# Kernel optimization log

Measured on AMD Instinct MI355X. Metric: run time of the kernel, lower is better.

## Reference

```python
import jax, jax.numpy as jnp
import numpy as np

N_U = 50000   # num user nodes
N_I = 50000   # num item nodes
D = 64        # in_size == out_size
H = 128       # SemanticAttention hidden size (default)
E = 500000    # edges per meta-path graph
NEG_SLOPE = 0.01


def setup_inputs() -> dict:
    key = jax.random.key(0)
    ks = jax.random.split(key, 24)
    rn = lambda k, shp, s=0.1: jax.random.normal(k, shp, jnp.float32) * s
    ri = lambda k, shp, n: jax.random.randint(k, shp, 0, n, dtype=jnp.int32)
    return dict(
        feat_user=rn(ks[0], (N_U, D)), feat_item=rn(ks[1], (N_I, D)),
        attn_l=rn(ks[2], (4, D)), attn_r=rn(ks[3], (4, D)),
        W_gc=rn(ks[4], (4, D, D)), b_gc=jnp.zeros((4, D), jnp.float32),
        sa_rel_W1=rn(ks[5], (D, H)), sa_rel_b1=jnp.zeros((H,), jnp.float32), sa_rel_w2=rn(ks[6], (H,)),
        sa_u_W1=rn(ks[7], (D, H)), sa_u_b1=jnp.zeros((H,), jnp.float32), sa_u_w2=rn(ks[8], (H,)),
        sa_i_W1=rn(ks[9], (D, H)), sa_i_b1=jnp.zeros((H,), jnp.float32), sa_i_w2=rn(ks[10], (H,)),
        rel_u_src=ri(ks[11], (2, E), N_I), rel_u_dst=ri(ks[12], (2, E), N_U),
        rel_i_src=ri(ks[13], (2, E), N_U), rel_i_dst=ri(ks[14], (2, E), N_I),
        mp_u_src=ri(ks[15], (2, E), N_U), mp_u_dst=ri(ks[16], (2, E), N_U),
        mp_i_src=ri(ks[17], (2, E), N_I), mp_i_dst=ri(ks[18], (2, E), N_I),
    )


def _edge_softmax(e, dst, n_dst):
    # segment-wise (per destination node) softmax over irregular edges
    m = jax.ops.segment_max(e, dst, num_segments=n_dst)
    ex = jnp.exp(e - m[dst])
    s = jax.ops.segment_sum(ex, dst, num_segments=n_dst)
    return ex / s[dst]


def _heco_gat(src, dst, feat_src, feat_dst, al, ar, n_dst):
    # HeCoGATConv: el = sum(ft_src*attn_l), er = sum(ft_dst*attn_r)
    el = feat_src @ al  # (N_src,)
    er = feat_dst @ ar  # (N_dst,)
    e = jax.nn.leaky_relu(el[src] + er[dst], NEG_SLOPE)  # (E,)
    a = _edge_softmax(e, dst, n_dst)
    out = jax.ops.segment_sum(feat_src[src] * a[:, None], dst, num_segments=n_dst)
    return jax.nn.elu(out)


def _graph_conv(src, dst, feat, W, b, n):
    # DGL GraphConv with norm='both', activation=elu
    ones = jnp.ones(src.shape, jnp.float32)
    deg_out = jax.ops.segment_sum(ones, src, num_segments=n)
    deg_in = jax.ops.segment_sum(ones, dst, num_segments=n)
    no = jnp.where(deg_out > 0, deg_out, 1.0) ** -0.5
    ni = jnp.where(deg_in > 0, deg_in, 1.0) ** -0.5
    h = feat * no[:, None]
    agg = jax.ops.segment_sum(h[src], dst, num_segments=n)
    agg = agg * ni[:, None]
    return jax.nn.elu(agg @ W + b)


def _semantic_attention(z, W1, b1, w2):
    # z: (N, M, D) -> (N, D)
    w = (jnp.tanh(z @ W1 + b1) @ w2).mean(0)  # (M,)
    beta = jax.nn.softmax(w)
    return jnp.einsum('nmd,m->nd', z, beta)


def reference(feat_user, feat_item, attn_l, attn_r, W_gc, b_gc,
              sa_rel_W1, sa_rel_b1, sa_rel_w2,
              sa_u_W1, sa_u_b1, sa_u_w2,
              sa_i_W1, sa_i_b1, sa_i_w2,
              rel_u_src, rel_u_dst, rel_i_src, rel_i_dst,
              mp_u_src, mp_u_dst, mp_i_src, mp_i_dst):
    # --- RelationalAGG: HeCo GAT over schema-level relations ---
    zu = jnp.stack([
        _heco_gat(rel_u_src[0], rel_u_dst[0], feat_item, feat_user, attn_l[0], attn_r[0], N_U),
        _heco_gat(rel_u_src[1], rel_u_dst[1], feat_item, feat_user, attn_l[1], attn_r[1], N_U),
    ], axis=1)  # (N_U, 2, D)
    rel_u = _semantic_attention(zu, sa_rel_W1, sa_rel_b1, sa_rel_w2)
    zi = jnp.stack([
        _heco_gat(rel_i_src[0], rel_i_dst[0], feat_user, feat_item, attn_l[2], attn_r[2], N_I),
        _heco_gat(rel_i_src[1], rel_i_dst[1], feat_user, feat_item, attn_l[3], attn_r[3], N_I),
    ], axis=1)
    rel_i = _semantic_attention(zi, sa_rel_W1, sa_rel_b1, sa_rel_w2)
    # --- HAN layers: GraphConv over meta-path reachable graphs ---
    hu = jnp.stack([
        _graph_conv(mp_u_src[0], mp_u_dst[0], feat_user, W_gc[0], b_gc[0], N_U),
        _graph_conv(mp_u_src[1], mp_u_dst[1], feat_user, W_gc[1], b_gc[1], N_U),
    ], axis=1)
    han_u = _semantic_attention(hu, sa_u_W1, sa_u_b1, sa_u_w2)
    hi = jnp.stack([
        _graph_conv(mp_i_src[0], mp_i_dst[0], feat_item, W_gc[2], b_gc[2], N_I),
        _graph_conv(mp_i_src[1], mp_i_dst[1], feat_item, W_gc[3], b_gc[3], N_I),
    ], axis=1)
    han_i = _semantic_attention(hi, sa_i_W1, sa_i_b1, sa_i_w2)
    user_emb = rel_u + han_u
    item_emb = rel_i + han_i
    return jnp.concatenate([user_emb, item_emb], axis=0)  # (N_U + N_I, D)
```

## Files before the change

kernel.cpp:

```cpp
#include <hip/hip_runtime.h>
#include <math.h>

#define NU 50000
#define NI 50000
#define NN 50000
#define DD 64
#define HHID 128
#define EE 500000
#define NEG_SLOPE 0.01f
#define NBKT 196
#define CAP 3072
#define TILE 8192
#define TPG 62
#define P1T 512
#define NIMG 12
#define AGGB 1563
#define SEMB 512

typedef _Float16 half_t;
typedef _Float16 half8 __attribute__((ext_vector_type(8)));
typedef float f32x4 __attribute__((ext_vector_type(4)));
union H4 { uint2 u; half_t h[4]; };
union H8 { uint4 u; half_t h[8]; };
union HS { half8 h; int i[4]; uint4 u; };
union HC { unsigned short us; half_t h; };

struct Ptr4c { const float* p[4]; };
struct Ptr4m { float*       p[4]; };
struct EdgeArgs { const int* src[8]; const int* dst[8]; };
struct GatArgs { const half_t* fsrc[4]; half_t* zout[4]; };
struct GcArgs  { const half_t* feat[4]; half_t* hout[4]; };
struct WArgs   { const float* el[4]; const float* er[4]; const int* deg_src; };
struct SemArgs { const half_t* z[4]; const float* W1[4]; const float* b1[4]; const float* w2[4]; };
struct PrepArgs {
    const float* featI; const float* featU;
    Ptr4c vi; Ptr4c vu; Ptr4m oi; Ptr4m ou;
    half_t* FBI; half_t* FBU;
    const float* W_gc; half_t* W16;
};

__global__ __launch_bounds__(256) void prep_kernel(PrepArgs pa) {
    int b = blockIdx.x;
    int t = threadIdx.x;
    if (b == 6250) {
        int g = t >> 6;
        int lane = t & 63;
        int cl = lane & 15, quad = lane >> 4;
#pragma unroll
        for (int nt = 0; nt < 4; nt++) {
#pragma unroll
            for (int kh = 0; kh < 2; kh++) {
                H8 o;
#pragma unroll
                for (int j = 0; j < 8; j++) {
                    int k = kh * 32 + quad * 8 + j;
                    int n = nt * 16 + cl;
                    o.h[j] = (half_t)pa.W_gc[g * 4096 + k * 64 + n];
                }
                *(uint4*)(pa.W16 + ((g * 8 + nt * 2 + kh) * 64 + lane) * 8) = o.u;
            }
        }
        return;
    }
    const float* feat; Ptr4c vecs; Ptr4m outs; half_t* fb16; int bb;
    if (b < 3125) { feat = pa.featI; vecs = pa.vi; outs = pa.oi; fb16 = pa.FBI; bb = b; }
    else          { feat = pa.featU; vecs = pa.vu; outs = pa.ou; fb16 = pa.FBU; bb = b - 3125; }
    int w = bb * 4 + (t >> 6);
    int lane = t & 63;
    int sub = lane >> 4, r = lane & 15;
    int node = w * 4 + sub;
    float4 f = *(const float4*)(feat + node * DD + r * 4);
    H4 o16;
    o16.h[0] = (half_t)f.x; o16.h[1] = (half_t)f.y; o16.h[2] = (half_t)f.z; o16.h[3] = (half_t)f.w;
    *(uint2*)(fb16 + node * DD + r * 4) = o16.u;
#pragma unroll
    for (int j = 0; j < 4; j++) {
        float4 vv = *(const float4*)(vecs.p[j] + r * 4);
        float val = f.x * vv.x + f.y * vv.y + f.z * vv.z + f.w * vv.w;
        val += __shfl_down(val, 8);
        val += __shfl_down(val, 4);
        val += __shfl_down(val, 2);
        val += __shfl_down(val, 1);
        if (r == 0) outs.p[j][node] = val;
    }
}

__global__ __launch_bounds__(P1T) void part1_kernel(EdgeArgs a, int* __restrict__ ccnt,
                                                    int* __restrict__ coarse) {
    __shared__ int bc_cnt[256], bc_scan[256], bc_start[256], bc_cur[256], bc_gbase[256];
    __shared__ int stage[TILE];
    int t = threadIdx.x;
    int g = blockIdx.x / TPG;
    int tile = blockIdx.x % TPG;
    int e0 = tile * TILE;
    int tile_n = min(TILE, EE - e0);
    bool cnt_only = g >= 8;
    const int* gk = (cnt_only ? a.src[g - 4] : a.dst[g]) + e0;
    const int* gs = cnt_only ? gk : (a.src[g] + e0);
    if (t < 256) bc_cnt[t] = 0;
    __syncthreads();
    for (int pos = t * 4; pos < tile_n; pos += P1T * 4) {
        int4 k4 = *(const int4*)(gk + pos);
        atomicAdd(&bc_cnt[k4.x >> 8], 1);
        atomicAdd(&bc_cnt[k4.y >> 8], 1);
        atomicAdd(&bc_cnt[k4.z >> 8], 1);
        atomicAdd(&bc_cnt[k4.w >> 8], 1);
    }
    __syncthreads();
    if (t < 256) bc_scan[t] = bc_cnt[t];
    __syncthreads();
    for (int off = 1; off < 256; off <<= 1) {
        int v = (t < 256 && t >= off) ? bc_scan[t - off] : 0;
        __syncthreads();
        if (t < 256) bc_scan[t] += v;
        __syncthreads();
    }
    if (t < 256) {
        int st = bc_scan[t] - bc_cnt[t];
        bc_start[t] = st;
        bc_cur[t] = st;
        bc_gbase[t] = (t < NBKT && bc_cnt[t] > 0) ? atomicAdd(&ccnt[g * NBKT + t], bc_cnt[t]) : 0;
    }
    __syncthreads();
    for (int pos = t * 4; pos < tile_n; pos += P1T * 4) {
        int4 k4 = *(const int4*)(gk + pos);
        int4 s4;
        if (cnt_only) { s4 = make_int4(0, 0, 0, 0); }
        else          { s4 = *(const int4*)(gs + pos); }
        int b0 = k4.x >> 8, b1 = k4.y >> 8, b2 = k4.z >> 8, b3 = k4.w >> 8;
        int sl0 = atomicAdd(&bc_cur[b0], 1);
        int sl1 = atomicAdd(&bc_cur[b1], 1);
        int sl2 = atomicAdd(&bc_cur[b2], 1);
        int sl3 = atomicAdd(&bc_cur[b3], 1);
        stage[sl0] = s4.x | ((k4.x & 255) << 16) | (b0 << 24);
        stage[sl1] = s4.y | ((k4.y & 255) << 16) | (b1 << 24);
        stage[sl2] = s4.z | ((k4.z & 255) << 16) | (b2 << 24);
        stage[sl3] = s4.w | ((k4.w & 255) << 16) | (b3 << 24);
    }
    __syncthreads();
    for (int j = t; j < tile_n; j += P1T) {
        int p = stage[j];
        int b = (unsigned)p >> 24;
        int pos = bc_gbase[b] + (j - bc_start[b]);
        if (pos < CAP) coarse[(g * NBKT + b) * CAP + pos] = p & 0x00FFFFFF;
    }
}

__global__ __launch_bounds__(256) void degcnt_kernel(const int* __restrict__ ccnt,
                                                     const int* __restrict__ coarse,
                                                     int* __restrict__ DEG_SRC) {
    __shared__ int cnt[256];
    int t = threadIdx.x;
    int g2 = blockIdx.x / NBKT;
    int b = blockIdx.x % NBKT;
    int img = 8 + g2;
    int n = min(ccnt[img * NBKT + b], CAP);
    cnt[t] = 0;
    __syncthreads();
    const int* pairs = coarse + (img * NBKT + b) * CAP;
    for (int i = t; i < n; i += 256) atomicAdd(&cnt[(pairs[i] >> 16) & 255], 1);
    __syncthreads();
    int v = (b << 8) + t;
    if (v < NN) DEG_SRC[g2 * NN + v] = cnt[t];
}

__global__ __launch_bounds__(256) void part2_kernel(const int* __restrict__ ccnt,
                                                    const int* __restrict__ coarse,
                                                    WArgs wa,
                                                    int* __restrict__ bucket,
                                                    int2* __restrict__ RD) {
    __shared__ int sb[256];
    __shared__ int cnt5[256], off5[256], s2[256];
    __shared__ int ordered[CAP];
    int t = threadIdx.x;
    int g = blockIdx.x / NBKT;
    int b = blockIdx.x % NBKT;
    int ccv = (t < NBKT) ? min(ccnt[g * NBKT + t], CAP) : 0;
    sb[t] = ccv;
    cnt5[t] = 0;
    __syncthreads();
    for (int off = 1; off < 256; off <<= 1) {
        int vv = (t >= off) ? sb[t - off] : 0;
        __syncthreads();
        sb[t] += vv;
        __syncthreads();
    }
    int base = (b > 0) ? sb[b - 1] : 0;
    int n = sb[b] - base;
    int node0 = b << 8;
    const int* pairs = coarse + (g * NBKT + b) * CAP;
    for (int i = t; i < n; i += 256) atomicAdd(&cnt5[pairs[i] >> 16], 1);
    __syncthreads();
    int myc = cnt5[t];
    s2[t] = myc;
    __syncthreads();
    for (int off = 1; off < 256; off <<= 1) {
        int vv = (t >= off) ? s2[t - off] : 0;
        __syncthreads();
        s2[t] += vv;
        __syncthreads();
    }
    int ex = s2[t] - myc;
    off5[t] = ex;
    int v = node0 + t;
    if (v < NN) RD[g * NN + v] = make_int2(base + ex, myc);
    __syncthreads();
    int nm1 = n - 1;
    for (int ib = t; ib < n; ib += 1024) {
        int p[4];
#pragma unroll
        for (int u = 0; u < 4; u++) {
            int i = ib + u * 256;
            p[u] = pairs[(i < n) ? i : nm1];
        }
        float w[4];
        if (g < 4) {
            float a0[4], a1[4];
#pragma unroll
            for (int u = 0; u < 4; u++) a0[u] = wa.el[g][p[u] & 0xFFFF];
#pragma unroll
            for (int u = 0; u < 4; u++) a1[u] = wa.er[g][node0 + (p[u] >> 16)];
#pragma unroll
            for (int u = 0; u < 4; u++) {
                float e = a0[u] + a1[u];
                e = (e >= 0.f) ? e : NEG_SLOPE * e;
                w[u] = __expf(e);
            }
        } else {
            int dv[4];
#pragma unroll
            for (int u = 0; u < 4; u++) dv[u] = wa.deg_src[(g - 4) * NN + (p[u] & 0xFFFF)];
#pragma unroll
            for (int u = 0; u < 4; u++) w[u] = __builtin_amdgcn_rsqf((float)dv[u]);
        }
#pragma unroll
        for (int u = 0; u < 4; u++) {
            int i = ib + u * 256;
            if (i < n) {
                HC cv; cv.h = (half_t)w[u];
                int slot = atomicAdd(&off5[p[u] >> 16], 1);
                ordered[slot] = (p[u] & 0xFFFF) | ((int)cv.us << 16);
            }
        }
    }
    __syncthreads();
    int* bko = bucket + g * EE + base;
    for (int i = t; i < n; i += 256) bko[i] = ordered[i];
}

__global__ __launch_bounds__(256) void agg_kernel(GatArgs ga, GcArgs gc, half_t* __restrict__ AGG,
                                                  const int2* __restrict__ RD,
                                                  const int* __restrict__ bucket) {
    int g = blockIdx.x / AGGB;
    int nb = blockIdx.x % AGGB;
    int t = threadIdx.x;
    int wv = t >> 6, lane = t & 63;
    int q = lane >> 3, r = lane & 7;
    int v = nb * 32 + wv * 8 + q;
    bool vok = v < NN;
    int2 rd = RD[g * NN + (vok ? v : 0)];
    int start = rd.x;
    int dg = vok ? rd.y : 0;
    const int* bk = bucket + g * EE;
    const half_t* feat = (g < 4) ? ga.fsrc[g] : gc.feat[g - 4];
    int roff = r << 3;
    int obase = lane & 56;
    HS acc[4];
#pragma unroll
    for (int a = 0; a < 4; a++)
#pragma unroll
        for (int j = 0; j < 4; j++) acc[a].i[j] = 0;
    float s_l = 0.f;
    for (int b8 = 0; b8 < dg; b8 += 8) {
        int rem = dg - b8;
        int p = bk[start + b8 + ((r < rem) ? r : 0)];
#pragma unroll
        for (int j = 0; j < 8; j++) {
            if (j < rem) {
                int pj = __shfl(p, obase + j);
                HC wj; wj.us = (unsigned short)((unsigned)pj >> 16);
                s_l += (float)wj.h;
                HS row; row.u = *(const uint4*)(feat + (((pj & 0xFFFF) << 6) + roff));
                half_t wh = wj.h;
                half8 ws = {wh, wh, wh, wh, wh, wh, wh, wh};
                acc[j & 3].h += row.h * ws;
            }
        }
    }
    acc[0].h += acc[1].h;
    acc[2].h += acc[3].h;
    acc[0].h += acc[2].h;
    if (g < 4) {
        float inv = (dg > 0) ? __builtin_amdgcn_rcpf(s_l) : 0.f;
        H8 o;
#pragma unroll
        for (int i = 0; i < 8; i++) {
            float x = (float)acc[0].h[i] * inv;
            x = (x > 0.f) ? x : (__expf(x) - 1.f);
            o.h[i] = (half_t)x;
        }
        if (vok) *(uint4*)(ga.zout[g] + (v << 7) + roff) = o.u;
    } else {
        float niv = (dg > 0) ? __builtin_amdgcn_rsqf((float)dg) : 1.0f;
        H8 o;
#pragma unroll
        for (int i = 0; i < 8; i++) o.h[i] = (half_t)((float)acc[0].h[i] * niv);
        if (vok) *(uint4*)(AGG + (((g - 4) * NN + v) << 6) + roff) = o.u;
    }
}

__global__ __launch_bounds__(256) void trans_kernel(GcArgs gc, const half_t* __restrict__ AGG,
                                                    const half_t* __restrict__ W16,
                                                    const float* __restrict__ b_gc) {
    int t = threadIdx.x;
    int wv = t >> 6, lane = t & 63;
    int g = blockIdx.x / 782;
    int tile = (blockIdx.x % 782) * 4 + wv;
    if (tile >= 3125) return;
    int cl = lane & 15, quad = lane >> 4;
    const half_t* ab = AGG + ((g * NN + tile * 16 + cl) << 6);
    half8 A0 = *(const half8*)(ab + quad * 8);
    half8 A1 = *(const half8*)(ab + 32 + quad * 8);
    const half_t* wbase = W16 + g * 8 * 64 * 8;
    half_t* hout = gc.hout[g];
#pragma unroll
    for (int nt = 0; nt < 4; nt++) {
        float bb = b_gc[g * 64 + nt * 16 + cl];
        f32x4 c = {bb, bb, bb, bb};
        half8 B0 = *(const half8*)(wbase + ((nt * 2 + 0) * 64 + lane) * 8);
        half8 B1 = *(const half8*)(wbase + ((nt * 2 + 1) * 64 + lane) * 8);
        c = __builtin_amdgcn_mfma_f32_16x16x32_f16(A0, B0, c, 0, 0, 0);
        c = __builtin_amdgcn_mfma_f32_16x16x32_f16(A1, B1, c, 0, 0, 0);
#pragma unroll
        for (int r_ = 0; r_ < 4; r_++) {
            int node = tile * 16 + quad * 4 + r_;
            float x = c[r_];
            x = (x > 0.f) ? x : (__expf(x) - 1.f);
            hout[node * 128 + nt * 16 + cl] = (half_t)x;
        }
    }
}

__global__ __launch_bounds__(256) void sem_att_kernel(SemArgs sa, float* __restrict__ wsum) {
    __shared__ float s0[4], s1[4];
    int inst = blockIdx.x / SEMB;
    int blk  = blockIdx.x % SEMB;
    int t = threadIdx.x;
    int wv = t >> 6, lane = t & 63;
    int quad = lane >> 4, cl = lane & 15;
    const half_t* z = sa.z[inst];
    const float* W1 = sa.W1[inst];
    half8 Bf[2][2];
    float b1v[2], w2v[2];
#pragma unroll
    for (int u = 0; u < 2; u++) {
        int nt = wv * 2 + u;
        int n = nt * 16 + cl;
#pragma unroll
        for (int kh = 0; kh < 2; kh++) {
#pragma unroll
            for (int j = 0; j < 8; j++) {
                int k = kh * 32 + quad * 8 + j;
                Bf[u][kh][j] = (half_t)W1[k * HHID + n];
            }
        }
        b1v[u] = sa.b1[inst][nt * 16 + cl];
        w2v[u] = sa.w2[inst][nt * 16 + cl];
    }
    float local0 = 0.f, local1 = 0.f;
    int tile = blk;
    half8 A0, A1, nA0, nA1;
    {
        int m = (tile >= 3125) ? 1 : 0;
        int node = (tile - m * 3125) * 16 + cl;
        const half_t* zr = z + node * 128 + m * 64 + quad * 8;
        A0 = *(const half8*)(zr);
        A1 = *(const half8*)(zr + 32);
    }
    while (tile < 6250) {
        int ntile = tile + SEMB;
        if (ntile < 6250) {
            int m = (ntile >= 3125) ? 1 : 0;
            int node = (ntile - m * 3125) * 16 + cl;
            const half_t* zr = z + node * 128 + m * 64 + quad * 8;
            nA0 = *(const half8*)(zr);
            nA1 = *(const half8*)(zr + 32);
        }
        float sumv = 0.f;
#pragma unroll
        for (int u = 0; u < 2; u++) {
            f32x4 c = {0.f, 0.f, 0.f, 0.f};
            c = __builtin_amdgcn_mfma_f32_16x16x32_f16(A0, Bf[u][0], c, 0, 0, 0);
            c = __builtin_amdgcn_mfma_f32_16x16x32_f16(A1, Bf[u][1], c, 0, 0, 0);
#pragma unroll
            for (int r = 0; r < 4; r++) {
                float xv = c[r] + b1v[u];
                float tv = __expf(2.f * xv);
                float th = 1.f - 2.f * __builtin_amdgcn_rcpf(tv + 1.f);
                sumv += th * w2v[u];
            }
        }
#pragma unroll
        for (int off = 32; off > 0; off >>= 1) sumv += __shfl_down(sumv, off);
        if (lane == 0) { if (tile < 3125) local0 += sumv; else local1 += sumv; }
        A0 = nA0; A1 = nA1;
        tile = ntile;
    }
    if (lane == 0) { s0[wv] = local0; s1[wv] = local1; }
    __syncthreads();
    if (t == 0) {
        float a0 = s0[0] + s0[1] + s0[2] + s0[3];
        float a1 = s1[0] + s1[1] + s1[2] + s1[3];
        if (a0 != 0.f) atomicAdd(&wsum[inst * 2 + 0], a0);
        if (a1 != 0.f) atomicAdd(&wsum[inst * 2 + 1], a1);
    }
}

__global__ void combine_kernel(const half_t* __restrict__ ZU, const half_t* __restrict__ ZI,
                               const half_t* __restrict__ HU, const half_t* __restrict__ HI,
                               const float* __restrict__ wsum, float* __restrict__ out) {
    int gid = blockIdx.x * blockDim.x + threadIdx.x;
    if (gid >= (NU + NI) * 16) return;
    int node = gid >> 4;
    int c4 = (gid & 15) * 4;
    const half_t* zb; const half_t* hb;
    float wr0, wr1, wh0, wh1;
    int idx;
    if (node < NU) {
        zb = ZU; hb = HU; idx = node;
        wr0 = wsum[0]; wr1 = wsum[1]; wh0 = wsum[4]; wh1 = wsum[5];
    } else {
        zb = ZI; hb = HI; idx = node - NU;
        wr0 = wsum[2]; wr1 = wsum[3]; wh0 = wsum[6]; wh1 = wsum[7];
    }
    const float inv_n = 1.0f / 50000.0f;
    wr0 *= inv_n; wr1 *= inv_n; wh0 *= inv_n; wh1 *= inv_n;
    float m = fmaxf(wr0, wr1);
    float e0 = __expf(wr0 - m), e1 = __expf(wr1 - m);
    float br0 = e0 / (e0 + e1), br1 = e1 / (e0 + e1);
    m = fmaxf(wh0, wh1);
    e0 = __expf(wh0 - m); e1 = __expf(wh1 - m);
    float bh0 = e0 / (e0 + e1), bh1 = e1 / (e0 + e1);
    H4 z0, z1, h0, h1;
    z0.u = *(const uint2*)(zb + idx * 128 + c4);
    z1.u = *(const uint2*)(zb + idx * 128 + 64 + c4);
    h0.u = *(const uint2*)(hb + idx * 128 + c4);
    h1.u = *(const uint2*)(hb + idx * 128 + 64 + c4);
    float4 o;
    o.x = (float)z0.h[0] * br0 + (float)z1.h[0] * br1 + (float)h0.h[0] * bh0 + (float)h1.h[0] * bh1;
    o.y = (float)z0.h[1] * br0 + (float)z1.h[1] * br1 + (float)h0.h[1] * bh0 + (float)h1.h[1] * bh1;
    o.z = (float)z0.h[2] * br0 + (float)z1.h[2] * br1 + (float)h0.h[2] * bh0 + (float)h1.h[2] * bh1;
    o.w = (float)z0.h[3] * br0 + (float)z1.h[3] * br1 + (float)h0.h[3] * bh0 + (float)h1.h[3] * bh1;
    *(float4*)(out + node * 64 + c4) = o;
}

extern "C" void kernel_launch(void* const* d_in, const int* in_sizes, int n_in,
                              void* d_out, int out_size, void* d_ws, size_t ws_size,
                              hipStream_t stream) {
    const float* feat_user = (const float*)d_in[0];
    const float* feat_item = (const float*)d_in[1];
    const float* attn_l    = (const float*)d_in[2];
    const float* attn_r    = (const float*)d_in[3];
    const float* W_gc      = (const float*)d_in[4];
    const float* b_gc      = (const float*)d_in[5];
    const float* sa_rel_W1 = (const float*)d_in[6];
    const float* sa_rel_b1 = (const float*)d_in[7];
    const float* sa_rel_w2 = (const float*)d_in[8];
    const float* sa_u_W1   = (const float*)d_in[9];
    const float* sa_u_b1   = (const float*)d_in[10];
    const float* sa_u_w2   = (const float*)d_in[11];
    const float* sa_i_W1   = (const float*)d_in[12];
    const float* sa_i_b1   = (const float*)d_in[13];
    const float* sa_i_w2   = (const float*)d_in[14];
    const int* rel_u_src = (const int*)d_in[15];
    const int* rel_u_dst = (const int*)d_in[16];
    const int* rel_i_src = (const int*)d_in[17];
    const int* rel_i_dst = (const int*)d_in[18];
    const int* mp_u_src  = (const int*)d_in[19];
    const int* mp_u_dst  = (const int*)d_in[20];
    const int* mp_i_src  = (const int*)d_in[21];
    const int* mp_i_dst  = (const int*)d_in[22];

    half_t* ZU   = (half_t*)d_ws;
    half_t* ZI   = ZU + NN * 128;
    half_t* HU   = ZI + NN * 128;
    half_t* HI   = HU + NN * 128;
    half_t* FBU  = HI + NN * 128;
    half_t* FBI  = FBU + NN * 64;
    float*  DI   = (float*)(FBI + NN * 64);
    float*  DU   = DI + 4 * NN;
    int2*   RD   = (int2*)(DU + 4 * NN);
    int*    BUCKET = (int*)(RD + 8 * NN);
    int*    CCNT = BUCKET + 8 * EE;
    int*    DEG_SRC = CCNT + 12 * 256;
    float*  WSUM = (float*)(DEG_SRC + 4 * NN);
    half_t* W16  = (half_t*)(WSUM + 8);
    half_t* AGG  = W16 + 4 * 4096;
    int*    COARSE = (int*)d_ws;

    hipMemsetAsync(CCNT, 0, (size_t)(12 * 256 + 4 * NN) * sizeof(int) + 8 * sizeof(float), stream);

    PrepArgs pa;
    pa.featI = feat_item; pa.featU = feat_user;
    pa.vi = Ptr4c{{ attn_l + 0 * DD, attn_l + 1 * DD, attn_r + 2 * DD, attn_r + 3 * DD }};
    pa.oi = Ptr4m{{ DI, DI + NI, DI + 2 * NI, DI + 3 * NI }};
    pa.vu = Ptr4c{{ attn_l + 2 * DD, attn_l + 3 * DD, attn_r + 0 * DD, attn_r + 1 * DD }};
    pa.ou = Ptr4m{{ DU, DU + NU, DU + 2 * NU, DU + 3 * NU }};
    pa.FBI = FBI; pa.FBU = FBU;
    pa.W_gc = W_gc; pa.W16 = W16;
    prep_kernel<<<6251, 256, 0, stream>>>(pa);

    EdgeArgs ea;
    ea.src[0] = rel_u_src;      ea.dst[0] = rel_u_dst;
    ea.src[1] = rel_u_src + EE; ea.dst[1] = rel_u_dst + EE;
    ea.src[2] = rel_i_src;      ea.dst[2] = rel_i_dst;
    ea.src[3] = rel_i_src + EE; ea.dst[3] = rel_i_dst + EE;
    ea.src[4] = mp_u_src;       ea.dst[4] = mp_u_dst;
    ea.src[5] = mp_u_src + EE;  ea.dst[5] = mp_u_dst + EE;
    ea.src[6] = mp_i_src;       ea.dst[6] = mp_i_dst;
    ea.src[7] = mp_i_src + EE;  ea.dst[7] = mp_i_dst + EE;

    part1_kernel<<<NIMG * TPG, P1T, 0, stream>>>(ea, CCNT, COARSE);
    degcnt_kernel<<<4 * NBKT, 256, 0, stream>>>(CCNT, COARSE, DEG_SRC);

    WArgs wa;
    wa.el[0] = DI;      wa.er[0] = DU + 2 * NU;
    wa.el[1] = DI + NI; wa.er[1] = DU + 3 * NU;
    wa.el[2] = DU;      wa.er[2] = DI + 2 * NI;
    wa.el[3] = DU + NU; wa.er[3] = DI + 3 * NI;
    wa.deg_src = DEG_SRC;
    part2_kernel<<<8 * NBKT, 256, 0, stream>>>(CCNT, COARSE, wa, BUCKET, RD);

    GatArgs ga;
    ga.fsrc[0] = FBI; ga.zout[0] = ZU;
    ga.fsrc[1] = FBI; ga.zout[1] = ZU + 64;
    ga.fsrc[2] = FBU; ga.zout[2] = ZI;
    ga.fsrc[3] = FBU; ga.zout[3] = ZI + 64;
    GcArgs gc;
    gc.feat[0] = FBU; gc.hout[0] = HU;
    gc.feat[1] = FBU; gc.hout[1] = HU + 64;
    gc.feat[2] = FBI; gc.hout[2] = HI;
    gc.feat[3] = FBI; gc.hout[3] = HI + 64;
    agg_kernel<<<8 * AGGB, 256, 0, stream>>>(ga, gc, AGG, RD, BUCKET);

    trans_kernel<<<4 * 782, 256, 0, stream>>>(gc, AGG, W16, b_gc);

    SemArgs sa;
    sa.z[0] = ZU; sa.W1[0] = sa_rel_W1; sa.b1[0] = sa_rel_b1; sa.w2[0] = sa_rel_w2;
    sa.z[1] = ZI; sa.W1[1] = sa_rel_W1; sa.b1[1] = sa_rel_b1; sa.w2[1] = sa_rel_w2;
    sa.z[2] = HU; sa.W1[2] = sa_u_W1;   sa.b1[2] = sa_u_b1;   sa.w2[2] = sa_u_w2;
    sa.z[3] = HI; sa.W1[3] = sa_i_W1;   sa.b1[3] = sa_i_b1;   sa.w2[3] = sa_i_w2;
    sem_att_kernel<<<4 * SEMB, 256, 0, stream>>>(sa, WSUM);

    combine_kernel<<<((NU + NI) * 16 + 255) / 256, 256, 0, stream>>>(ZU, ZI, HU, HI, WSUM, (float*)d_out);
}
```

Before: 347.3 us.

## Stage semantic-attention input tiles through LDS with async global_load_lds double buffering

```diff
diff --git a/kernel.cpp b/kernel.cpp
--- a/kernel.cpp
+++ b/kernel.cpp
@@ -342,6 +342,7 @@
 }
 
 __global__ __launch_bounds__(256) void sem_att_kernel(SemArgs sa, float* __restrict__ wsum) {
+    __shared__ half_t As[2][1024];
     __shared__ float s0[4], s1[4];
     int inst = blockIdx.x / SEMB;
     int blk  = blockIdx.x % SEMB;
@@ -368,24 +369,37 @@
         w2v[u] = sa.w2[inst][nt * 16 + cl];
     }
     float local0 = 0.f, local1 = 0.f;
+
+#define SEM_STAGE(buf, tp) { \
+    if (wv < 2) { \
+        int m_ = ((tp) >= 3125) ? 1 : 0; \
+        int tm_ = (tp) - m_ * 3125; \
+        int c_ = (wv << 6) + lane; \
+        int n_ = c_ >> 3, j_ = c_ & 7; \
+        const half_t* src_ = z + (size_t)(tm_ * 16 + n_) * 128 + m_ * 64 + j_ * 8; \
+        __builtin_amdgcn_global_load_lds( \
+            (const __attribute__((address_space(1))) unsigned int*)src_, \
+            (__attribute__((address_space(3))) unsigned int*)(&As[buf][wv * 512]), \
+            16, 0, 0); \
+    } }
+
     int tile = blk;
-    half8 A0, A1, nA0, nA1;
-    {
-        int m = (tile >= 3125) ? 1 : 0;
-        int node = (tile - m * 3125) * 16 + cl;
-        const half_t* zr = z + node * 128 + m * 64 + quad * 8;
-        A0 = *(const half8*)(zr);
-        A1 = *(const half8*)(zr + 32);
-    }
+    int cur = 0;
+    SEM_STAGE(0, tile);
     while (tile < 6250) {
         int ntile = tile + SEMB;
-        if (ntile < 6250) {
-            int m = (ntile >= 3125) ? 1 : 0;
-            int node = (ntile - m * 3125) * 16 + cl;
-            const half_t* zr = z + node * 128 + m * 64 + quad * 8;
-            nA0 = *(const half8*)(zr);
-            nA1 = *(const half8*)(zr + 32);
-        }
+        bool more = ntile < 6250;
+        if (more) {
+            SEM_STAGE(cur ^ 1, ntile);
+            asm volatile("s_waitcnt vmcnt(1)" ::: "memory");
+        } else {
+            asm volatile("s_waitcnt vmcnt(0)" ::: "memory");
+        }
+        __builtin_amdgcn_sched_barrier(0);
+        __builtin_amdgcn_s_barrier();
+        const half_t* ar = &As[cur][cl * 64 + quad * 8];
+        half8 A0 = *(const half8*)(ar);
+        half8 A1 = *(const half8*)(ar + 32);
         float sumv = 0.f;
 #pragma unroll
         for (int u = 0; u < 2; u++) {
@@ -395,16 +409,21 @@
 #pragma unroll
             for (int r = 0; r < 4; r++) {
                 float xv = c[r] + b1v[u];
-                float tv = __expf(2.f * xv);
-                float th = 1.f - 2.f * __builtin_amdgcn_rcpf(tv + 1.f);
+                float ev = __expf(2.f * xv);
+                float th = 1.f - 2.f * __builtin_amdgcn_rcpf(ev + 1.f);
                 sumv += th * w2v[u];
             }
         }
-#pragma unroll
-        for (int off = 32; off > 0; off >>= 1) sumv += __shfl_down(sumv, off);
-        if (lane == 0) { if (tile < 3125) local0 += sumv; else local1 += sumv; }
-        A0 = nA0; A1 = nA1;
+        if (tile < 3125) local0 += sumv; else local1 += sumv;
+        __builtin_amdgcn_s_barrier();
+        cur ^= 1;
         tile = ntile;
+    }
+#undef SEM_STAGE
+#pragma unroll
+    for (int off = 32; off > 0; off >>= 1) {
+        local0 += __shfl_down(local0, off);
+        local1 += __shfl_down(local1, off);
     }
     if (lane == 0) { s0[wv] = local0; s1[wv] = local1; }
     __syncthreads();
```

Result: faster. 335.8 us (-3.3%).
